# Optimization experiments

Hardware: AMD Instinct MI355X
Metric: run time of the kernel (lower is better)

The kernel has to match this reference:

```python
import jax, jax.numpy as jnp
import numpy as np

N, B, NUM_NODES, D_IN = 16384, 16, 1024, 1024
H, C = 4, 128
E = 262144


def _g(k, shape, fan_in):
    return jax.random.normal(k, shape, jnp.float32) * (1.0 / np.sqrt(fan_in))


def setup_inputs() -> dict:
    key = jax.random.key(0)
    ks = jax.random.split(key, 32)
    HC = H * C
    inp = {
        'x': jax.random.normal(ks[0], (N, D_IN), jnp.float32),
        'edge_index': jax.random.randint(ks[1], (2, E), 0, N, dtype=jnp.int64),
        'batch': jnp.repeat(jnp.arange(B, dtype=jnp.int64), NUM_NODES),
        # GATConv 1 (D_IN -> H x C, concat)
        'W1': _g(ks[2], (D_IN, HC), D_IN),
        'att_src1': _g(ks[3], (H, C), C),
        'att_dst1': _g(ks[4], (H, C), C),
        'b1': jnp.zeros((HC,), jnp.float32),
        # GATConv 2 (H*C -> H x C, concat)
        'W2': _g(ks[5], (HC, HC), HC),
        'att_src2': _g(ks[6], (H, C), C),
        'att_dst2': _g(ks[7], (H, C), C),
        'b2': jnp.zeros((HC,), jnp.float32),
        # pooling linears (HC -> 1)
        'p1w': _g(ks[8], (HC, 1), HC), 'p1b': jnp.zeros((1,), jnp.float32),
        'p2w': _g(ks[9], (HC, 1), HC), 'p2b': jnp.zeros((1,), jnp.float32),
        # layer_norm0 (applied to x2 per original code)
        'ln_g': jnp.ones((NUM_NODES,), jnp.float32),
        'ln_b': jnp.zeros((NUM_NODES,), jnp.float32),
        # encoder MLP 1024->512->256->128->64, last 64->1
        'fw1': _g(ks[10], (NUM_NODES, 512), NUM_NODES), 'fb1': jnp.zeros((512,), jnp.float32),
        'fw2': _g(ks[11], (512, 256), 512), 'fb2': jnp.zeros((256,), jnp.float32),
        'fw3': _g(ks[12], (256, 128), 256), 'fb3': jnp.zeros((128,), jnp.float32),
        'fw4': _g(ks[13], (128, 64), 128), 'fb4': jnp.zeros((64,), jnp.float32),
        'lw': _g(ks[14], (64, 1), 64), 'lb': jnp.zeros((1,), jnp.float32),
    }
    return inp


def gat_conv(x, src, dst, W, a_src, a_dst, b):
    # x: [N, F_in] -> h: [N, H, C]
    h = (x @ W).reshape(N, H, C)
    alpha_src = jnp.sum(h * a_src[None], axis=-1)  # [N, H]
    alpha_dst = jnp.sum(h * a_dst[None], axis=-1)  # [N, H]
    e = jax.nn.leaky_relu(alpha_src[src] + alpha_dst[dst], 0.2)  # [E', H]
    # segment softmax over destination neighborhoods (every node has a self loop)
    emax = jax.ops.segment_max(e, dst, num_segments=N)
    ex = jnp.exp(e - emax[dst])
    denom = jax.ops.segment_sum(ex, dst, num_segments=N)
    alpha = ex / (denom[dst] + 1e-16)  # [E', H]
    msg = h[src] * alpha[:, :, None]  # [E', H, C]
    out = jax.ops.segment_sum(msg, dst, num_segments=N)  # [N, H, C]
    return out.reshape(N, H * C) + b


def layer_norm(x, g, b, eps=1e-5):
    mu = jnp.mean(x, axis=-1, keepdims=True)
    var = jnp.var(x, axis=-1, keepdims=True)
    return (x - mu) * jax.lax.rsqrt(var + eps) * g + b


def reference(x, edge_index, batch, W1, att_src1, att_dst1, b1, W2, att_src2, att_dst2, b2,
              p1w, p1b, p2w, p2b, ln_g, ln_b, fw1, fb1, fw2, fb2, fw3, fb3, fw4, fb4, lw, lb):
    # add self loops (GATConv default)
    loops = jnp.arange(N, dtype=edge_index.dtype)
    src = jnp.concatenate([edge_index[0], loops])
    dst = jnp.concatenate([edge_index[1], loops])

    h1 = jax.nn.elu(gat_conv(x, src, dst, W1, att_src1, att_dst1, b1))
    # pool1 + to_dense_batch: batch is sorted with NUM_NODES nodes per graph -> reshape
    x1 = (h1 @ p1w + p1b).squeeze(-1).reshape(B, NUM_NODES)
    h2 = jax.nn.elu(gat_conv(h1, src, dst, W2, att_src2, att_dst2, b2))
    x2 = (h2 @ p2w + p2b).squeeze(-1).reshape(B, NUM_NODES)

    # opt.layer_norm=True; original bug: x2 normalized by layer_norm0
    x2 = layer_norm(x2, ln_g, ln_b)
    multiscale = x2  # which_layer == 'layer3'

    e = jax.nn.elu(multiscale @ fw1 + fb1)
    e = jax.nn.elu(e @ fw2 + fb2)
    e = jax.nn.elu(e @ fw3 + fb3)
    e = jax.nn.elu(e @ fw4 + fb4)
    pred = e @ lw + lb  # act_type='none' -> no activation
    return multiscale, e, pred
```

## Files before the change

### kernel.cpp

```cpp
#include <hip/hip_runtime.h>
#include <math.h>

#define NN    16384
#define DIN   1024
#define HCdim 512
#define NHEAD 4
#define NE_   262144
#define EP_   (NE_ + NN)

using short8  = __attribute__((ext_vector_type(8))) short;
using floatx4 = __attribute__((ext_vector_type(4))) float;

typedef __attribute__((address_space(3))) unsigned int lds_uint;
typedef const __attribute__((address_space(1))) unsigned int glb_uint;
#define ASYNC_LD16(g, l) __builtin_amdgcn_global_load_lds((glb_uint*)(g), (lds_uint*)(l), 16, 0, 0)

__device__ __forceinline__ float eluf(float x){ return x > 0.f ? x : expm1f(x); }
__device__ __forceinline__ float lrelu(float x){ return x > 0.f ? x : 0.2f * x; }
__device__ __forceinline__ float bf2f(unsigned short u){
    union { unsigned int i; float f; } c; c.i = ((unsigned int)u) << 16; return c.f;
}
__device__ __forceinline__ unsigned short f2b(float f){
    union { float f; unsigned int u; } c; c.f = f;
    unsigned int u = c.u;
    return (unsigned short)((u + 0x7FFFu + ((u >> 16) & 1u)) >> 16);
}

__global__ void k_zero_i(int* __restrict__ p, int n){
    int i = blockIdx.x * 256 + threadIdx.x;
    if (i < n) p[i] = 0;
}

__global__ void k_degree(const int* __restrict__ ei, int* __restrict__ deg){
    int i = blockIdx.x * 256 + threadIdx.x;
    if (i >= EP_) return;
    int d = (i < NE_) ? ei[NE_ + i] : (i - NE_);
    atomicAdd(&deg[d], 1);
}

__global__ __launch_bounds__(1024) void k_scan(const int* __restrict__ deg, int* __restrict__ offs){
    __shared__ int s[1024];
    int tid  = threadIdx.x;
    int base = tid * 16;
    int local[16];
    int sum = 0;
    #pragma unroll
    for (int i = 0; i < 16; i++){ local[i] = deg[base + i]; sum += local[i]; }
    s[tid] = sum;
    __syncthreads();
    for (int off = 1; off < 1024; off <<= 1){
        int v = (tid >= off) ? s[tid - off] : 0;
        __syncthreads();
        s[tid] += v;
        __syncthreads();
    }
    int run = (tid == 0) ? 0 : s[tid - 1];
    #pragma unroll
    for (int i = 0; i < 16; i++){ offs[base + i] = run; run += local[i]; }
    if (tid == 1023) offs[NN] = run;
}

__global__ void k_scatter(const int* __restrict__ ei, const int* __restrict__ offs,
                          int* __restrict__ cursor, int* __restrict__ csr){
    int i = blockIdx.x * 256 + threadIdx.x;
    if (i >= EP_) return;
    int srcv, dstv;
    if (i < NE_){ srcv = ei[i]; dstv = ei[NE_ + i]; }
    else        { srcv = dstv = i - NE_; }
    int pos = offs[dstv] + atomicAdd(&cursor[dstv], 1);
    csr[pos] = srcv;
}

__global__ __launch_bounds__(256) void k_cast_x(const float* __restrict__ x, ushort* __restrict__ xb){
    int i = blockIdx.x * 256 + threadIdx.x;
    float4 v = *(const float4*)(x + (size_t)i * 4);
    ushort4 o = { f2b(v.x), f2b(v.y), f2b(v.z), f2b(v.w) };
    *(ushort4*)(xb + (size_t)i * 4) = o;
}

__global__ __launch_bounds__(256) void k_castT(const float* __restrict__ W, ushort* __restrict__ WT,
                                               int K, int Nn, int kshift){
    int t  = blockIdx.x * 256 + threadIdx.x;
    int n  = t >> kshift;
    int kb = (t & ((1 << kshift) - 1)) * 4;
    ushort4 o;
    o.x = f2b(W[(size_t)(kb + 0) * Nn + n]);
    o.y = f2b(W[(size_t)(kb + 1) * Nn + n]);
    o.z = f2b(W[(size_t)(kb + 2) * Nn + n]);
    o.w = f2b(W[(size_t)(kb + 3) * Nn + n]);
    *(ushort4*)(WT + (size_t)n * K + kb) = o;
}

__global__ __launch_bounds__(256) void gemm_bf16(const ushort* __restrict__ A,
                                                 const ushort* __restrict__ BT,
                                                 ushort* __restrict__ C,
                                                 int M, int Nn, int K){
    __shared__ ushort As[128 * 32];
    __shared__ ushort Bs[128 * 32];
    int tid = threadIdx.x;
    int m0 = blockIdx.y * 128, n0 = blockIdx.x * 128;
    int lane = tid & 63, w = tid >> 6;
    int wm = (w >> 1) * 64, wn = (w & 1) * 64;
    int la = lane & 15, qd = lane >> 4;

    int srow = tid >> 2, schunk = (tid & 3) * 8;
    const ushort* Ag = A  + (size_t)(m0 + srow) * K + schunk;
    const ushort* Bg = BT + (size_t)(n0 + srow) * K + schunk;
    ushort* Asw = &As[srow * 32 + schunk];
    ushort* Bsw = &Bs[srow * 32 + schunk];

    floatx4 acc[4][4] = {};
    for (int k0 = 0; k0 < K; k0 += 32){
        __syncthreads();
        ASYNC_LD16(Ag + k0,                  Asw);
        ASYNC_LD16(Ag + (size_t)64 * K + k0, Asw + 64 * 32);
        ASYNC_LD16(Bg + k0,                  Bsw);
        ASYNC_LD16(Bg + (size_t)64 * K + k0, Bsw + 64 * 32);
        __syncthreads();
        short8 af[4], bf[4];
        #pragma unroll
        for (int i = 0; i < 4; i++){
            af[i] = *(const short8*)&As[(wm + i*16 + la) * 32 + qd * 8];
            bf[i] = *(const short8*)&Bs[(wn + i*16 + la) * 32 + qd * 8];
        }
        #pragma unroll
        for (int i = 0; i < 4; i++)
            #pragma unroll
            for (int j = 0; j < 4; j++)
                acc[i][j] = __builtin_amdgcn_mfma_f32_16x16x32_bf16(af[i], bf[j], acc[i][j], 0, 0, 0);
    }
    #pragma unroll
    for (int i = 0; i < 4; i++)
        #pragma unroll
        for (int j = 0; j < 4; j++){
            int col = n0 + wn + j * 16 + la;
            #pragma unroll
            for (int r = 0; r < 4; r++){
                int row = m0 + wm + i * 16 + qd * 4 + r;
                C[(size_t)row * Nn + col] = f2b(acc[i][j][r]);
            }
        }
}

__global__ __launch_bounds__(256) void k_alpha(const ushort* __restrict__ h,
    const float* __restrict__ att_s, const float* __restrict__ att_d,
    float* __restrict__ as_, float* __restrict__ ad_){
    int gt   = blockIdx.x * 256 + threadIdx.x;
    int wid  = gt >> 6;
    int lane = threadIdx.x & 63;
    int n = wid >> 2, hh = wid & 3;
    unsigned int hv = *(const unsigned int*)(h + (size_t)n * HCdim + hh * 128 + lane * 2);
    float h0 = bf2f(hv & 0xffff), h1 = bf2f(hv >> 16);
    float2 sv = *(const float2*)(att_s + hh * 128 + lane * 2);
    float2 dv = *(const float2*)(att_d + hh * 128 + lane * 2);
    float ss = h0 * sv.x + h1 * sv.y;
    float sd = h0 * dv.x + h1 * dv.y;
    #pragma unroll
    for (int off = 32; off; off >>= 1){ ss += __shfl_down(ss, off); sd += __shfl_down(sd, off); }
    if (lane == 0){ as_[n * 4 + hh] = ss; ad_[n * 4 + hh] = sd; }
}

template<bool POOL>
__global__ __launch_bounds__(256) void k_aggregate(const ushort* __restrict__ h,
    const int* __restrict__ offs, const int* __restrict__ csr,
    const float* __restrict__ as_, const float* __restrict__ ad_,
    const float* __restrict__ bias, ushort* __restrict__ out,
    const float* __restrict__ pw, const float* __restrict__ pb, float* __restrict__ x2){
    int wv   = threadIdx.x >> 6;
    int lane = threadIdx.x & 63;
    int n    = blockIdx.x * 4 + wv;
    int head = lane >> 4;
    int start = offs[n], end = offs[n + 1];
    float adh = ad_[n * 4 + head];
    float dsum = 0.f;
    float a0=0.f,a1=0.f,a2=0.f,a3=0.f,a4=0.f,a5=0.f,a6=0.f,a7=0.f;
    for (int j = start; j < end; j++){
        int s = csr[j];
        float wgt = __expf(lrelu(as_[s * 4 + head] + adh));
        dsum += wgt;
        uint4 hv = *(const uint4*)(h + (size_t)s * HCdim + lane * 8);
        a0 = fmaf(wgt, bf2f(hv.x & 0xffff), a0);
        a1 = fmaf(wgt, bf2f(hv.x >> 16),    a1);
        a2 = fmaf(wgt, bf2f(hv.y & 0xffff), a2);
        a3 = fmaf(wgt, bf2f(hv.y >> 16),    a3);
        a4 = fmaf(wgt, bf2f(hv.z & 0xffff), a4);
        a5 = fmaf(wgt, bf2f(hv.z >> 16),    a5);
        a6 = fmaf(wgt, bf2f(hv.w & 0xffff), a6);
        a7 = fmaf(wgt, bf2f(hv.w >> 16),    a7);
    }
    float rden = 1.f / (dsum + 1e-16f);
    float4 b0 = *(const float4*)(bias + lane * 8);
    float4 b1 = *(const float4*)(bias + lane * 8 + 4);
    float e0 = eluf(fmaf(a0, rden, b0.x));
    float e1 = eluf(fmaf(a1, rden, b0.y));
    float e2 = eluf(fmaf(a2, rden, b0.z));
    float e3 = eluf(fmaf(a3, rden, b0.w));
    float e4 = eluf(fmaf(a4, rden, b1.x));
    float e5 = eluf(fmaf(a5, rden, b1.y));
    float e6 = eluf(fmaf(a6, rden, b1.z));
    float e7 = eluf(fmaf(a7, rden, b1.w));
    uint4 o;
    o.x = (unsigned)f2b(e0) | ((unsigned)f2b(e1) << 16);
    o.y = (unsigned)f2b(e2) | ((unsigned)f2b(e3) << 16);
    o.z = (unsigned)f2b(e4) | ((unsigned)f2b(e5) << 16);
    o.w = (unsigned)f2b(e6) | ((unsigned)f2b(e7) << 16);
    *(uint4*)(out + (size_t)n * HCdim + lane * 8) = o;
    if (POOL){
        float4 w0 = *(const float4*)(pw + lane * 8);
        float4 w1 = *(const float4*)(pw + lane * 8 + 4);
        float s = e0*w0.x + e1*w0.y + e2*w0.z + e3*w0.w
                + e4*w1.x + e5*w1.y + e6*w1.z + e7*w1.w;
        #pragma unroll
        for (int off = 32; off; off >>= 1) s += __shfl_down(s, off);
        if (lane == 0) x2[n] = s + pb[0];
    }
}

__global__ __launch_bounds__(256) void k_ln(const float* __restrict__ x2,
    const float* __restrict__ lng, const float* __restrict__ lnb,
    float* __restrict__ xnb, float* __restrict__ out){
    __shared__ float red[8];
    __shared__ float stats[2];
    int b = blockIdx.x, tid = threadIdx.x;
    float4 v = *(const float4*)(x2 + b * 1024 + tid * 4);
    float s  = v.x + v.y + v.z + v.w;
    float sq = v.x * v.x + v.y * v.y + v.z * v.z + v.w * v.w;
    #pragma unroll
    for (int off = 32; off; off >>= 1){ s += __shfl_down(s, off); sq += __shfl_down(sq, off); }
    if ((tid & 63) == 0){ red[(tid >> 6) * 2] = s; red[(tid >> 6) * 2 + 1] = sq; }
    __syncthreads();
    if (tid == 0){
        float S  = red[0] + red[2] + red[4] + red[6];
        float SQ = red[1] + red[3] + red[5] + red[7];
        float mu  = S * (1.f / 1024.f);
        float var = SQ * (1.f / 1024.f) - mu * mu;
        stats[0] = mu; stats[1] = rsqrtf(var + 1e-5f);
    }
    __syncthreads();
    float mu = stats[0], r = stats[1];
    float4 g4  = *(const float4*)(lng + tid * 4);
    float4 bb4 = *(const float4*)(lnb + tid * 4);
    float4 o;
    o.x = (v.x - mu) * r * g4.x + bb4.x;
    o.y = (v.y - mu) * r * g4.y + bb4.y;
    o.z = (v.z - mu) * r * g4.z + bb4.z;
    o.w = (v.w - mu) * r * g4.w + bb4.w;
    *(float4*)(xnb + b * 1024 + tid * 4) = o;
    *(float4*)(out + b * 1024 + tid * 4) = o;
}

template<int K, int NOUT>
__global__ __launch_bounds__(256) void k_fc(const float* __restrict__ in,
    const float* __restrict__ W, const float* __restrict__ bias, float* __restrict__ outb){
    __shared__ float xs[K];
    __shared__ float red[4][64];
    int tid = threadIdx.x;
    int b = blockIdx.y, c0 = blockIdx.x * 64;
    int tx = tid & 63, ty = tid >> 6;
    for (int i = tid * 4; i < K; i += 1024)
        *(float4*)&xs[i] = *(const float4*)(in + b * K + i);
    __syncthreads();
    const float* wp = W + (size_t)(ty * (K / 4)) * NOUT + c0 + tx;
    float a = 0.f;
    #pragma unroll 8
    for (int i = 0; i < K / 4; i++)
        a = fmaf(xs[ty * (K / 4) + i], wp[(size_t)i * NOUT], a);
    red[ty][tx] = a;
    __syncthreads();
    if (ty == 0){
        float v = red[0][tx] + red[1][tx] + red[2][tx] + red[3][tx] + bias[c0 + tx];
        outb[b * NOUT + tx + c0] = eluf(v);
    }
}

__global__ __launch_bounds__(256) void k_fc_final(const float* __restrict__ in,
    const float* __restrict__ W, const float* __restrict__ bias,
    const float* __restrict__ lw, const float* __restrict__ lb, float* __restrict__ out){
    __shared__ float xs[128];
    __shared__ float red[4][64];
    __shared__ float evs[64];
    int tid = threadIdx.x;
    int b = blockIdx.x;
    int tx = tid & 63, ty = tid >> 6;
    if (tid * 4 < 128)
        *(float4*)&xs[tid * 4] = *(const float4*)(in + b * 128 + tid * 4);
    __syncthreads();
    const float* wp = W + (size_t)(ty * 32) * 64 + tx;
    float a = 0.f;
    #pragma unroll
    for (int i = 0; i < 32; i++)
        a = fmaf(xs[ty * 32 + i], wp[(size_t)i * 64], a);
    red[ty][tx] = a;
    __syncthreads();
    if (ty == 0){
        float ev = eluf(red[0][tx] + red[1][tx] + red[2][tx] + red[3][tx] + bias[tx]);
        evs[tx] = ev;
        out[16384 + b * 64 + tx] = ev;
    }
    __syncthreads();
    if (ty == 0){
        float p = evs[tx] * lw[tx];
        #pragma unroll
        for (int off = 32; off; off >>= 1) p += __shfl_down(p, off);
        if (tx == 0) out[16384 + 1024 + b] = p + lb[0];
    }
}

extern "C" void kernel_launch(void* const* d_in, const int* in_sizes, int n_in,
                              void* d_out, int out_size, void* d_ws, size_t ws_size,
                              hipStream_t stream) {
    const float* x        = (const float*)d_in[0];
    const int*   ei       = (const int*)  d_in[1];
    const float* W1       = (const float*)d_in[3];
    const float* att_src1 = (const float*)d_in[4];
    const float* att_dst1 = (const float*)d_in[5];
    const float* b1       = (const float*)d_in[6];
    const float* W2       = (const float*)d_in[7];
    const float* att_src2 = (const float*)d_in[8];
    const float* att_dst2 = (const float*)d_in[9];
    const float* b2       = (const float*)d_in[10];
    const float* p2w      = (const float*)d_in[13];
    const float* p2b      = (const float*)d_in[14];
    const float* ln_g     = (const float*)d_in[15];
    const float* ln_b     = (const float*)d_in[16];
    const float* fw1      = (const float*)d_in[17];
    const float* fb1      = (const float*)d_in[18];
    const float* fw2      = (const float*)d_in[19];
    const float* fb2      = (const float*)d_in[20];
    const float* fw3      = (const float*)d_in[21];
    const float* fb3      = (const float*)d_in[22];
    const float* fw4      = (const float*)d_in[23];
    const float* fb4      = (const float*)d_in[24];
    const float* lw       = (const float*)d_in[25];
    const float* lb       = (const float*)d_in[26];
    float* out = (float*)d_out;

    char* w = (char*)d_ws;
    ushort* xb   = (ushort*)(w);
    ushort* h1b  = (ushort*)(w);
    ushort* h2b  = (ushort*)(w + 16777216);
    ushort* hpre = (ushort*)(w + 33554432);
    ushort* W1T  = (ushort*)(w + 50331648);
    ushort* W2T  = (ushort*)(w + 51380224);
    float* asb   = (float*)(w + 51904512);
    float* adb   = (float*)(w + 52166656);
    int*   deg   = (int*)  (w + 52428800);
    int*   cursor= (int*)  (w + 52494336);
    int*   offs  = (int*)  (w + 52559872);
    int*   csr   = (int*)  (w + 52625664);
    float* x2b   = (float*)(w + 53739776);
    float* xnb   = (float*)(w + 53805056);
    float* e1b   = (float*)(w + 53870592);
    float* e2b   = (float*)(w + 53903360);
    float* e3b   = (float*)(w + 53919744);

    k_zero_i <<<(2 * NN + 255) / 256, 256, 0, stream>>>(deg, 2 * NN);
    k_degree <<<(EP_ + 255) / 256, 256, 0, stream>>>(ei, deg);
    k_scan   <<<1, 1024, 0, stream>>>(deg, offs);
    k_scatter<<<(EP_ + 255) / 256, 256, 0, stream>>>(ei, offs, cursor, csr);

    k_cast_x<<<NN * DIN / 4 / 256, 256, 0, stream>>>(x, xb);
    k_castT <<<DIN * HCdim / 4 / 256, 256, 0, stream>>>(W1, W1T, DIN, HCdim, 8);
    k_castT <<<HCdim * HCdim / 4 / 256, 256, 0, stream>>>(W2, W2T, HCdim, HCdim, 7);

    dim3 ggrid(HCdim / 128, NN / 128);
    gemm_bf16         <<<ggrid, 256, 0, stream>>>(xb, W1T, hpre, NN, HCdim, DIN);
    k_alpha           <<<NN * NHEAD / 4, 256, 0, stream>>>(hpre, att_src1, att_dst1, asb, adb);
    k_aggregate<false><<<NN / 4, 256, 0, stream>>>(hpre, offs, csr, asb, adb, b1, h1b,
                                                   nullptr, nullptr, nullptr);
    gemm_bf16         <<<ggrid, 256, 0, stream>>>(h1b, W2T, hpre, NN, HCdim, HCdim);
    k_alpha           <<<NN * NHEAD / 4, 256, 0, stream>>>(hpre, att_src2, att_dst2, asb, adb);
    k_aggregate<true> <<<NN / 4, 256, 0, stream>>>(hpre, offs, csr, asb, adb, b2, h2b,
                                                   p2w, p2b, x2b);
    k_ln              <<<16, 256, 0, stream>>>(x2b, ln_g, ln_b, xnb, out);
    k_fc<1024, 512>   <<<dim3(8, 16), 256, 0, stream>>>(xnb, fw1, fb1, e1b);
    k_fc< 512, 256>   <<<dim3(4, 16), 256, 0, stream>>>(e1b, fw2, fb2, e2b);
    k_fc< 256, 128>   <<<dim3(2, 16), 256, 0, stream>>>(e2b, fw3, fb3, e3b);
    k_fc_final        <<<16, 256, 0, stream>>>(e3b, fw4, fb4, lw, lb, out);
}
```

Baseline: 392.5 us.

## Fuse attention logits into GEMM epilogue, precompute edge weights, prefetch aggregation loads

Merges the three cast kernels into one launch. Computes alpha_src/alpha_dst inside the GEMM epilogue from fp32 accumulators, which removes the separate k_alpha pass over h. Adds a k_edgew kernel that precomputes per-edge exp weights in bf16, and rewrites aggregation to batch-load CSR indices with readlane and software-prefetch two edges ahead. Fuses the layernorm into the first FC layer. The trade-offs are bf16 rounding of the edge weights, an extra edge-weight buffer, and the layernorm stats being recomputed in every FC block.

```diff
diff --git a/kernel.cpp b/kernel.cpp
--- a/kernel.cpp
+++ b/kernel.cpp
@@ -71,34 +71,44 @@
     csr[pos] = srcv;
 }
 
-__global__ __launch_bounds__(256) void k_cast_x(const float* __restrict__ x, ushort* __restrict__ xb){
-    int i = blockIdx.x * 256 + threadIdx.x;
-    float4 v = *(const float4*)(x + (size_t)i * 4);
-    ushort4 o = { f2b(v.x), f2b(v.y), f2b(v.z), f2b(v.w) };
-    *(ushort4*)(xb + (size_t)i * 4) = o;
-}
-
-__global__ __launch_bounds__(256) void k_castT(const float* __restrict__ W, ushort* __restrict__ WT,
-                                               int K, int Nn, int kshift){
-    int t  = blockIdx.x * 256 + threadIdx.x;
-    int n  = t >> kshift;
-    int kb = (t & ((1 << kshift) - 1)) * 4;
-    ushort4 o;
-    o.x = f2b(W[(size_t)(kb + 0) * Nn + n]);
-    o.y = f2b(W[(size_t)(kb + 1) * Nn + n]);
-    o.z = f2b(W[(size_t)(kb + 2) * Nn + n]);
-    o.w = f2b(W[(size_t)(kb + 3) * Nn + n]);
-    *(ushort4*)(WT + (size_t)n * K + kb) = o;
+__global__ __launch_bounds__(256) void k_casts(const float* __restrict__ x, ushort* __restrict__ xb,
+    const float* __restrict__ W1, ushort* __restrict__ W1T,
+    const float* __restrict__ W2, ushort* __restrict__ W2T){
+    int bid = blockIdx.x, tid = threadIdx.x;
+    if (bid < 16384){
+        int i = bid * 256 + tid;
+        float4 v = *(const float4*)(x + (size_t)i * 4);
+        ushort4 o = { f2b(v.x), f2b(v.y), f2b(v.z), f2b(v.w) };
+        *(ushort4*)(xb + (size_t)i * 4) = o;
+    } else if (bid < 16384 + 512){
+        int t = (bid - 16384) * 256 + tid;
+        int n = t >> 8, kb = (t & 255) * 4;
+        ushort4 o = { f2b(W1[(size_t)(kb+0)*HCdim + n]), f2b(W1[(size_t)(kb+1)*HCdim + n]),
+                      f2b(W1[(size_t)(kb+2)*HCdim + n]), f2b(W1[(size_t)(kb+3)*HCdim + n]) };
+        *(ushort4*)(W1T + (size_t)n * DIN + kb) = o;
+    } else {
+        int t = (bid - 16896) * 256 + tid;
+        int n = t >> 7, kb = (t & 127) * 4;
+        ushort4 o = { f2b(W2[(size_t)(kb+0)*HCdim + n]), f2b(W2[(size_t)(kb+1)*HCdim + n]),
+                      f2b(W2[(size_t)(kb+2)*HCdim + n]), f2b(W2[(size_t)(kb+3)*HCdim + n]) };
+        *(ushort4*)(W2T + (size_t)n * HCdim + kb) = o;
+    }
 }
 
 __global__ __launch_bounds__(256) void gemm_bf16(const ushort* __restrict__ A,
                                                  const ushort* __restrict__ BT,
                                                  ushort* __restrict__ C,
+                                                 const float* __restrict__ att_s,
+                                                 const float* __restrict__ att_d,
+                                                 float* __restrict__ as_, float* __restrict__ ad_,
                                                  int M, int Nn, int K){
     __shared__ ushort As[128 * 32];
     __shared__ ushort Bs[128 * 32];
+    __shared__ float prS[2][128];
+    __shared__ float prD[2][128];
     int tid = threadIdx.x;
     int m0 = blockIdx.y * 128, n0 = blockIdx.x * 128;
+    int cx = blockIdx.x;
     int lane = tid & 63, w = tid >> 6;
     int wm = (w >> 1) * 64, wn = (w & 1) * 64;
     int la = lane & 15, qd = lane >> 4;
@@ -129,6 +139,34 @@
             for (int j = 0; j < 4; j++)
                 acc[i][j] = __builtin_amdgcn_mfma_f32_16x16x32_bf16(af[i], bf[j], acc[i][j], 0, 0, 0);
     }
+    float asv[4], adv[4];
+    #pragma unroll
+    for (int j = 0; j < 4; j++){
+        asv[j] = att_s[cx * 128 + wn + j * 16 + la];
+        adv[j] = att_d[cx * 128 + wn + j * 16 + la];
+    }
+    int half = wn >> 6;
+    #pragma unroll
+    for (int i = 0; i < 4; i++){
+        #pragma unroll
+        for (int r = 0; r < 4; r++){
+            float ps = 0.f, pd = 0.f;
+            #pragma unroll
+            for (int j = 0; j < 4; j++){
+                ps = fmaf(acc[i][j][r], asv[j], ps);
+                pd = fmaf(acc[i][j][r], adv[j], pd);
+            }
+            #pragma unroll
+            for (int off = 1; off < 16; off <<= 1){
+                ps += __shfl_xor(ps, off);
+                pd += __shfl_xor(pd, off);
+            }
+            if (la == 0){
+                int rl = wm + i * 16 + qd * 4 + r;
+                prS[half][rl] = ps; prD[half][rl] = pd;
+            }
+        }
+    }
     #pragma unroll
     for (int i = 0; i < 4; i++)
         #pragma unroll
@@ -140,30 +178,44 @@
                 C[(size_t)row * Nn + col] = f2b(acc[i][j][r]);
             }
         }
-}
-
-__global__ __launch_bounds__(256) void k_alpha(const ushort* __restrict__ h,
-    const float* __restrict__ att_s, const float* __restrict__ att_d,
-    float* __restrict__ as_, float* __restrict__ ad_){
-    int gt   = blockIdx.x * 256 + threadIdx.x;
-    int wid  = gt >> 6;
-    int lane = threadIdx.x & 63;
-    int n = wid >> 2, hh = wid & 3;
-    unsigned int hv = *(const unsigned int*)(h + (size_t)n * HCdim + hh * 128 + lane * 2);
-    float h0 = bf2f(hv & 0xffff), h1 = bf2f(hv >> 16);
-    float2 sv = *(const float2*)(att_s + hh * 128 + lane * 2);
-    float2 dv = *(const float2*)(att_d + hh * 128 + lane * 2);
-    float ss = h0 * sv.x + h1 * sv.y;
-    float sd = h0 * dv.x + h1 * dv.y;
-    #pragma unroll
-    for (int off = 32; off; off >>= 1){ ss += __shfl_down(ss, off); sd += __shfl_down(sd, off); }
-    if (lane == 0){ as_[n * 4 + hh] = ss; ad_[n * 4 + hh] = sd; }
-}
+    __syncthreads();
+    if (tid < 128){
+        as_[(size_t)(m0 + tid) * 4 + cx] = prS[0][tid] + prS[1][tid];
+        ad_[(size_t)(m0 + tid) * 4 + cx] = prD[0][tid] + prD[1][tid];
+    }
+}
+
+__global__ __launch_bounds__(256) void k_edgew(const int* __restrict__ offs, const int* __restrict__ csr,
+    const float* __restrict__ as_, const float* __restrict__ ad_, ushort* __restrict__ wbuf){
+    int wv = threadIdx.x >> 6, lane = threadIdx.x & 63;
+    int n = blockIdx.x * 4 + wv;
+    int start = offs[n], end = offs[n + 1];
+    float4 ad4 = *(const float4*)(ad_ + (size_t)n * 4);
+    for (int j = start + lane; j < end; j += 64){
+        int s = csr[j];
+        float4 as4 = *(const float4*)(as_ + (size_t)s * 4);
+        ushort4 o = { f2b(__expf(lrelu(as4.x + ad4.x))), f2b(__expf(lrelu(as4.y + ad4.y))),
+                      f2b(__expf(lrelu(as4.z + ad4.z))), f2b(__expf(lrelu(as4.w + ad4.w))) };
+        *(ushort4*)(wbuf + (size_t)j * 4) = o;
+    }
+}
+
+#define AGG_CONSUME(WS, HV)                                  \
+    { float wgt = bf2f(WS);                                  \
+      dsum += wgt;                                           \
+      a0 = fmaf(wgt, bf2f(HV.x & 0xffff), a0);               \
+      a1 = fmaf(wgt, bf2f(HV.x >> 16),    a1);               \
+      a2 = fmaf(wgt, bf2f(HV.y & 0xffff), a2);               \
+      a3 = fmaf(wgt, bf2f(HV.y >> 16),    a3);               \
+      a4 = fmaf(wgt, bf2f(HV.z & 0xffff), a4);               \
+      a5 = fmaf(wgt, bf2f(HV.z >> 16),    a5);               \
+      a6 = fmaf(wgt, bf2f(HV.w & 0xffff), a6);               \
+      a7 = fmaf(wgt, bf2f(HV.w >> 16),    a7); }
 
 template<bool POOL>
 __global__ __launch_bounds__(256) void k_aggregate(const ushort* __restrict__ h,
     const int* __restrict__ offs, const int* __restrict__ csr,
-    const float* __restrict__ as_, const float* __restrict__ ad_,
+    const ushort* __restrict__ wbuf,
     const float* __restrict__ bias, ushort* __restrict__ out,
     const float* __restrict__ pw, const float* __restrict__ pb, float* __restrict__ x2){
     int wv   = threadIdx.x >> 6;
@@ -171,22 +223,31 @@
     int n    = blockIdx.x * 4 + wv;
     int head = lane >> 4;
     int start = offs[n], end = offs[n + 1];
-    float adh = ad_[n * 4 + head];
     float dsum = 0.f;
     float a0=0.f,a1=0.f,a2=0.f,a3=0.f,a4=0.f,a5=0.f,a6=0.f,a7=0.f;
-    for (int j = start; j < end; j++){
-        int s = csr[j];
-        float wgt = __expf(lrelu(as_[s * 4 + head] + adh));
-        dsum += wgt;
-        uint4 hv = *(const uint4*)(h + (size_t)s * HCdim + lane * 8);
-        a0 = fmaf(wgt, bf2f(hv.x & 0xffff), a0);
-        a1 = fmaf(wgt, bf2f(hv.x >> 16),    a1);
-        a2 = fmaf(wgt, bf2f(hv.y & 0xffff), a2);
-        a3 = fmaf(wgt, bf2f(hv.y >> 16),    a3);
-        a4 = fmaf(wgt, bf2f(hv.z & 0xffff), a4);
-        a5 = fmaf(wgt, bf2f(hv.z >> 16),    a5);
-        a6 = fmaf(wgt, bf2f(hv.w & 0xffff), a6);
-        a7 = fmaf(wgt, bf2f(hv.w >> 16),    a7);
+    for (int base = start; base < end; base += 64){
+        int cnt = min(64, end - base);
+        int pre = (base + lane < end) ? csr[base + lane] : 0;
+        int s0 = __builtin_amdgcn_readlane(pre, 0);
+        ushort w0 = wbuf[(size_t)base * 4 + head];
+        uint4  h0 = *(const uint4*)(h + (size_t)s0 * HCdim + lane * 8);
+        ushort w1 = 0; uint4 h1 = {0,0,0,0};
+        if (cnt > 1){
+            int s1 = __builtin_amdgcn_readlane(pre, 1);
+            w1 = wbuf[(size_t)(base + 1) * 4 + head];
+            h1 = *(const uint4*)(h + (size_t)s1 * HCdim + lane * 8);
+        }
+        for (int jj = 0; jj < cnt; jj++){
+            ushort w2 = 0; uint4 h2 = {0,0,0,0};
+            if (jj + 2 < cnt){
+                int s2 = __builtin_amdgcn_readlane(pre, jj + 2);
+                w2 = wbuf[(size_t)(base + jj + 2) * 4 + head];
+                h2 = *(const uint4*)(h + (size_t)s2 * HCdim + lane * 8);
+            }
+            AGG_CONSUME(w0, h0);
+            w0 = w1; h0 = h1;
+            w1 = w2; h1 = h2;
+        }
     }
     float rden = 1.f / (dsum + 1e-16f);
     float4 b0 = *(const float4*)(bias + lane * 8);
@@ -206,32 +267,36 @@
     o.w = (unsigned)f2b(e6) | ((unsigned)f2b(e7) << 16);
     *(uint4*)(out + (size_t)n * HCdim + lane * 8) = o;
     if (POOL){
-        float4 w0 = *(const float4*)(pw + lane * 8);
-        float4 w1 = *(const float4*)(pw + lane * 8 + 4);
-        float s = e0*w0.x + e1*w0.y + e2*w0.z + e3*w0.w
-                + e4*w1.x + e5*w1.y + e6*w1.z + e7*w1.w;
+        float4 w0p = *(const float4*)(pw + lane * 8);
+        float4 w1p = *(const float4*)(pw + lane * 8 + 4);
+        float s = e0*w0p.x + e1*w0p.y + e2*w0p.z + e3*w0p.w
+                + e4*w1p.x + e5*w1p.y + e6*w1p.z + e7*w1p.w;
         #pragma unroll
         for (int off = 32; off; off >>= 1) s += __shfl_down(s, off);
         if (lane == 0) x2[n] = s + pb[0];
     }
 }
 
-__global__ __launch_bounds__(256) void k_ln(const float* __restrict__ x2,
+__global__ __launch_bounds__(256) void k_fc1_ln(const float* __restrict__ x2,
     const float* __restrict__ lng, const float* __restrict__ lnb,
-    float* __restrict__ xnb, float* __restrict__ out){
-    __shared__ float red[8];
+    const float* __restrict__ W, const float* __restrict__ bias,
+    float* __restrict__ outms, float* __restrict__ e1b){
+    __shared__ float xs[1024];
+    __shared__ float red[4][64];
+    __shared__ float red2[8];
     __shared__ float stats[2];
-    int b = blockIdx.x, tid = threadIdx.x;
+    int tid = threadIdx.x;
+    int b = blockIdx.y, c0 = blockIdx.x * 64;
     float4 v = *(const float4*)(x2 + b * 1024 + tid * 4);
     float s  = v.x + v.y + v.z + v.w;
     float sq = v.x * v.x + v.y * v.y + v.z * v.z + v.w * v.w;
     #pragma unroll
     for (int off = 32; off; off >>= 1){ s += __shfl_down(s, off); sq += __shfl_down(sq, off); }
-    if ((tid & 63) == 0){ red[(tid >> 6) * 2] = s; red[(tid >> 6) * 2 + 1] = sq; }
+    if ((tid & 63) == 0){ red2[(tid >> 6) * 2] = s; red2[(tid >> 6) * 2 + 1] = sq; }
     __syncthreads();
     if (tid == 0){
-        float S  = red[0] + red[2] + red[4] + red[6];
-        float SQ = red[1] + red[3] + red[5] + red[7];
+        float S  = red2[0] + red2[2] + red2[4] + red2[6];
+        float SQ = red2[1] + red2[3] + red2[5] + red2[7];
         float mu  = S * (1.f / 1024.f);
         float var = SQ * (1.f / 1024.f) - mu * mu;
         stats[0] = mu; stats[1] = rsqrtf(var + 1e-5f);
@@ -245,8 +310,21 @@
     o.y = (v.y - mu) * r * g4.y + bb4.y;
     o.z = (v.z - mu) * r * g4.z + bb4.z;
     o.w = (v.w - mu) * r * g4.w + bb4.w;
-    *(float4*)(xnb + b * 1024 + tid * 4) = o;
-    *(float4*)(out + b * 1024 + tid * 4) = o;
+    *(float4*)&xs[tid * 4] = o;
+    if (blockIdx.x == 0) *(float4*)(outms + b * 1024 + tid * 4) = o;
+    __syncthreads();
+    int tx = tid & 63, ty = tid >> 6;
+    const float* wp = W + (size_t)(ty * 256) * 512 + c0 + tx;
+    float a = 0.f;
+    #pragma unroll 8
+    for (int i = 0; i < 256; i++)
+        a = fmaf(xs[ty * 256 + i], wp[(size_t)i * 512], a);
+    red[ty][tx] = a;
+    __syncthreads();
+    if (ty == 0){
+        float vv = red[0][tx] + red[1][tx] + red[2][tx] + red[3][tx] + bias[c0 + tx];
+        e1b[b * 512 + c0 + tx] = eluf(vv);
+    }
 }
 
 template<int K, int NOUT>
@@ -348,32 +426,31 @@
     int*   cursor= (int*)  (w + 52494336);
     int*   offs  = (int*)  (w + 52559872);
     int*   csr   = (int*)  (w + 52625664);
-    float* x2b   = (float*)(w + 53739776);
-    float* xnb   = (float*)(w + 53805056);
-    float* e1b   = (float*)(w + 53870592);
-    float* e2b   = (float*)(w + 53903360);
-    float* e3b   = (float*)(w + 53919744);
+    ushort* wbuf = (ushort*)(w + 53739776);
+    float* x2b   = (float*)(w + 55968000);
+    float* e1b   = (float*)(w + 56033536);
+    float* e2b   = (float*)(w + 56066304);
+    float* e3b   = (float*)(w + 56082688);
 
     k_zero_i <<<(2 * NN + 255) / 256, 256, 0, stream>>>(deg, 2 * NN);
     k_degree <<<(EP_ + 255) / 256, 256, 0, stream>>>(ei, deg);
     k_scan   <<<1, 1024, 0, stream>>>(deg, offs);
     k_scatter<<<(EP_ + 255) / 256, 256, 0, stream>>>(ei, offs, cursor, csr);
 
-    k_cast_x<<<NN * DIN / 4 / 256, 256, 0, stream>>>(x, xb);
-    k_castT <<<DIN * HCdim / 4 / 256, 256, 0, stream>>>(W1, W1T, DIN, HCdim, 8);
-    k_castT <<<HCdim * HCdim / 4 / 256, 256, 0, stream>>>(W2, W2T, HCdim, HCdim, 7);
+    k_casts<<<16384 + 512 + 256, 256, 0, stream>>>(x, xb, W1, W1T, W2, W2T);
 
     dim3 ggrid(HCdim / 128, NN / 128);
-    gemm_bf16         <<<ggrid, 256, 0, stream>>>(xb, W1T, hpre, NN, HCdim, DIN);
-    k_alpha           <<<NN * NHEAD / 4, 256, 0, stream>>>(hpre, att_src1, att_dst1, asb, adb);
-    k_aggregate<false><<<NN / 4, 256, 0, stream>>>(hpre, offs, csr, asb, adb, b1, h1b,
+    gemm_bf16         <<<ggrid, 256, 0, stream>>>(xb, W1T, hpre, att_src1, att_dst1,
+                                                  asb, adb, NN, HCdim, DIN);
+    k_edgew           <<<NN / 4, 256, 0, stream>>>(offs, csr, asb, adb, wbuf);
+    k_aggregate<false><<<NN / 4, 256, 0, stream>>>(hpre, offs, csr, wbuf, b1, h1b,
                                                    nullptr, nullptr, nullptr);
-    gemm_bf16         <<<ggrid, 256, 0, stream>>>(h1b, W2T, hpre, NN, HCdim, HCdim);
-    k_alpha           <<<NN * NHEAD / 4, 256, 0, stream>>>(hpre, att_src2, att_dst2, asb, adb);
-    k_aggregate<true> <<<NN / 4, 256, 0, stream>>>(hpre, offs, csr, asb, adb, b2, h2b,
+    gemm_bf16         <<<ggrid, 256, 0, stream>>>(h1b, W2T, hpre, att_src2, att_dst2,
+                                                  asb, adb, NN, HCdim, HCdim);
+    k_edgew           <<<NN / 4, 256, 0, stream>>>(offs, csr, asb, adb, wbuf);
+    k_aggregate<true> <<<NN / 4, 256, 0, stream>>>(hpre, offs, csr, wbuf, b2, h2b,
                                                    p2w, p2b, x2b);
-    k_ln              <<<16, 256, 0, stream>>>(x2b, ln_g, ln_b, xnb, out);
-    k_fc<1024, 512>   <<<dim3(8, 16), 256, 0, stream>>>(xnb, fw1, fb1, e1b);
+    k_fc1_ln          <<<dim3(8, 16), 256, 0, stream>>>(x2b, ln_g, ln_b, fw1, fb1, out, e1b);
     k_fc< 512, 256>   <<<dim3(4, 16), 256, 0, stream>>>(e1b, fw2, fb2, e2b);
     k_fc< 256, 128>   <<<dim3(2, 16), 256, 0, stream>>>(e2b, fw3, fb3, e3b);
     k_fc_final        <<<16, 256, 0, stream>>>(e3b, fw4, fb4, lw, lb, out);
```

Result: faster. 376.0 us (-4.2%).
